# Optimization experiments

Hardware: AMD Instinct MI355X
Metric: run time of the kernel (lower is better)

## Reference

```python
import jax, jax.numpy as jnp
import numpy as np

EPS = 1e-05

def setup_inputs() -> dict:
    key = jax.random.key(0)
    inputs = jax.random.normal(key, (32, 512, 768), dtype=jnp.float32)
    return {"inputs": inputs}

def reference(inputs) -> jnp.ndarray:
    # position weight: L2 norm per token, w[b,l] = sqrt(1e-5 + sum_d x^2)
    w = jnp.sqrt(EPS + jnp.sum(inputs * inputs, axis=-1))  # [B, L]
    # output[b,d,e] = sum_l w[b,l] * x[b,l,d] * x[b,l,e]
    # fused weighted Gram matrix; never materializes [B,L,D,D]
    return jnp.einsum('bld,ble->bde', inputs * w[..., None], inputs)
```

## Files before the change

kernel.cpp:

```cpp
#include <hip/hip_runtime.h>
#include <hip/hip_bf16.h>

#define BATCH 32
#define LL 512
#define DD 768
#define EPSC 1e-5f

typedef __attribute__((ext_vector_type(8))) short bf16x8;
typedef __attribute__((ext_vector_type(4))) float f32x4;

__global__ __launch_bounds__(256) void k_scales(const float* __restrict__ x,
                                                float* __restrict__ s) {
    int wave = threadIdx.x >> 6;
    int lane = threadIdx.x & 63;
    int row = blockIdx.x * 4 + wave;
    const float4* xr = (const float4*)(x + (size_t)row * DD);
    float sum = 0.f;
#pragma unroll
    for (int i = 0; i < 3; i++) {
        float4 v = xr[lane + i * 64];
        sum += v.x * v.x + v.y * v.y + v.z * v.z + v.w * v.w;
    }
#pragma unroll
    for (int off = 32; off > 0; off >>= 1)
        sum += __shfl_xor(sum, off, 64);
    if (lane == 0) s[row] = sqrtf(sqrtf(EPSC + sum));
}

__global__ __launch_bounds__(256) void k_transpose(const float* __restrict__ x,
                                                   const float* __restrict__ s,
                                                   ushort* __restrict__ yt) {
    __shared__ float tile[64][65];
    __shared__ float svec[64];
    int b = blockIdx.z;
    int l0 = blockIdx.y * 64;
    int d0 = blockIdx.x * 64;
    int t = threadIdx.x;
    if (t < 64) svec[t] = s[b * LL + l0 + t];
    const float* xp = x + ((size_t)b * LL + l0) * DD + d0;
    int f = t & 15, lr0 = t >> 4;
#pragma unroll
    for (int r = 0; r < 4; r++) {
        int l = lr0 + r * 16;
        float4 v = *(const float4*)(xp + (size_t)l * DD + f * 4);
#pragma unroll
        for (int j = 0; j < 4; j++)
            tile[l][f * 4 + j] = ((const float*)&v)[j];
    }
    __syncthreads();
    ushort* yp = yt + ((size_t)b * DD + d0) * LL + l0;
    int lc = t & 7, dl0 = t >> 3;
#pragma unroll
    for (int it = 0; it < 2; it++) {
        int d = dl0 + it * 32;
        bf16x8 w;
#pragma unroll
        for (int j = 0; j < 8; j++) {
            int l = lc * 8 + j;
            float v = tile[l][d] * svec[l];
            __hip_bfloat16 h = __float2bfloat16(v);
            w[j] = *(short*)&h;
        }
        *(bf16x8*)(yp + (size_t)d * LL + lc * 8) = w;
    }
}

__global__ __launch_bounds__(256) void k_gemm(const ushort* __restrict__ yt,
                                              float* __restrict__ out) {
    __shared__ ushort At[2][64 * 32];
    __shared__ ushort Bt[2][64 * 32];
    int i = blockIdx.x;
    int xcd = i & 7, slot = i >> 3;
    int b = xcd + 8 * (slot / 78);
    int p = slot % 78;
    int t = p, tm = 0, rem = 12;
    while (t >= rem) { t -= rem; rem--; tm++; }
    int tn = tm + t;
    bool diag = (tm == tn);
    int m0 = tm * 64, n0 = tn * 64;
    int tid = threadIdx.x;
    int wave = tid >> 6, lane = tid & 63;
    int wr = wave >> 1, wc = wave & 1;
    const ushort* yb = yt + (size_t)b * DD * LL;

    f32x4 acc[2][2];
#pragma unroll
    for (int ii = 0; ii < 2; ii++)
#pragma unroll
        for (int j = 0; j < 2; j++) acc[ii][j] = (f32x4){0.f, 0.f, 0.f, 0.f};

    int srow = lane >> 2;
    int ssw = (srow ^ (srow >> 1)) & 3;
    int scol = ((lane & 3) ^ ssw) * 8;
    int rloc = wave * 16 + srow;
    const ushort* gA = yb + (size_t)(m0 + rloc) * LL + scol;
    const ushort* gB = yb + (size_t)(n0 + rloc) * LL + scol;
    int fr = lane & 15;
    int fsw = (fr ^ (fr >> 1)) & 3;
    int fslot = (lane >> 4) ^ fsw;

#define STAGE(buf, ks) do {                                                   \
        int k0_ = (ks) * 32;                                                  \
        __builtin_amdgcn_global_load_lds(                                     \
            (const __attribute__((address_space(1))) void*)(gA + k0_),        \
            (__attribute__((address_space(3))) void*)(At[buf] + wave * 16 * 32), \
            16, 0, 0);                                                        \
        if (!diag)                                                            \
            __builtin_amdgcn_global_load_lds(                                 \
                (const __attribute__((address_space(1))) void*)(gB + k0_),    \
                (__attribute__((address_space(3))) void*)(Bt[buf] + wave * 16 * 32), \
                16, 0, 0);                                                    \
    } while (0)

    STAGE(0, 0);
    __syncthreads();
    for (int ks = 0; ks < 16; ks++) {
        int cur = ks & 1;
        if (ks < 15) STAGE(cur ^ 1, ks + 1);
        const ushort* Ab = At[cur];
        const ushort* Bb = diag ? At[cur] : Bt[cur];
        bf16x8 afrag[2], bfrag[2];
#pragma unroll
        for (int ii = 0; ii < 2; ii++) {
            int m = wr * 32 + ii * 16 + fr;
            afrag[ii] = *(const bf16x8*)(Ab + m * 32 + fslot * 8);
            int n = wc * 32 + ii * 16 + fr;
            bfrag[ii] = *(const bf16x8*)(Bb + n * 32 + fslot * 8);
        }
#pragma unroll
        for (int ii = 0; ii < 2; ii++)
#pragma unroll
            for (int j = 0; j < 2; j++)
                acc[ii][j] = __builtin_amdgcn_mfma_f32_16x16x32_bf16(
                    afrag[ii], bfrag[j], acc[ii][j], 0, 0, 0);
        if (ks < 15) __syncthreads();
    }
#undef STAGE

    float* op = out + (size_t)b * DD * DD;
#pragma unroll
    for (int ii = 0; ii < 2; ii++) {
        int colb = m0 + wr * 32 + ii * 16 + (lane >> 4) * 4;
#pragma unroll
        for (int j = 0; j < 2; j++) {
            int row = n0 + wc * 32 + j * 16 + fr;
            float4 v = {acc[ii][j][0], acc[ii][j][1], acc[ii][j][2], acc[ii][j][3]};
            *(float4*)(op + (size_t)row * DD + colb) = v;
        }
    }
    if (!diag) {
#pragma unroll
        for (int ii = 0; ii < 2; ii++) {
            int mbase = m0 + wr * 32 + ii * 16 + (lane >> 4) * 4;
#pragma unroll
            for (int j = 0; j < 2; j++) {
                int n = n0 + wc * 32 + j * 16 + fr;
#pragma unroll
                for (int r = 0; r < 4; r++)
                    op[(size_t)(mbase + r) * DD + n] = acc[ii][j][r];
            }
        }
    }
}

extern "C" void kernel_launch(void* const* d_in, const int* in_sizes, int n_in,
                              void* d_out, int out_size, void* d_ws, size_t ws_size,
                              hipStream_t stream) {
    const float* x = (const float*)d_in[0];
    float* s = (float*)d_ws;
    ushort* yt = (ushort*)((char*)d_ws + 65536);

    k_scales<<<dim3((BATCH * LL) / 4), 256, 0, stream>>>(x, s);
    k_transpose<<<dim3(DD / 64, LL / 64, BATCH), 256, 0, stream>>>(x, s, yt);
    k_gemm<<<dim3(78 * BATCH), 256, 0, stream>>>(yt, (float*)d_out);
}
```

Measured before the change: 137.8 us.

## Fuse norm and transpose kernels; double GEMM K-tile to 64

The row-norm scale computation is merged into the transpose kernel. Each block now handles 64 tokens across all 768 features, computing the scales locally and looping over 12 feature tiles. The GEMM K-step grows from 32 to 64 with a new XOR swizzle, which halves the number of barriers and loop iterations. The risk is the prep kernel: it drops to only 256 blocks, each running a long serial loop, which lowers parallelism.

```diff
diff --git a/kernel.cpp b/kernel.cpp
--- a/kernel.cpp
+++ b/kernel.cpp
@@ -9,66 +9,66 @@
 typedef __attribute__((ext_vector_type(8))) short bf16x8;
 typedef __attribute__((ext_vector_type(4))) float f32x4;
 
-__global__ __launch_bounds__(256) void k_scales(const float* __restrict__ x,
-                                                float* __restrict__ s) {
-    int wave = threadIdx.x >> 6;
-    int lane = threadIdx.x & 63;
-    int row = blockIdx.x * 4 + wave;
-    const float4* xr = (const float4*)(x + (size_t)row * DD);
-    float sum = 0.f;
-#pragma unroll
-    for (int i = 0; i < 3; i++) {
-        float4 v = xr[lane + i * 64];
-        sum += v.x * v.x + v.y * v.y + v.z * v.z + v.w * v.w;
-    }
-#pragma unroll
-    for (int off = 32; off > 0; off >>= 1)
-        sum += __shfl_xor(sum, off, 64);
-    if (lane == 0) s[row] = sqrtf(sqrtf(EPSC + sum));
-}
-
-__global__ __launch_bounds__(256) void k_transpose(const float* __restrict__ x,
-                                                   const float* __restrict__ s,
-                                                   ushort* __restrict__ yt) {
+__global__ __launch_bounds__(256) void k_prep(const float* __restrict__ x,
+                                              ushort* __restrict__ yt) {
     __shared__ float tile[64][65];
     __shared__ float svec[64];
-    int b = blockIdx.z;
-    int l0 = blockIdx.y * 64;
-    int d0 = blockIdx.x * 64;
+    int lb = blockIdx.x;
+    int b = blockIdx.y;
+    int l0 = lb * 64;
     int t = threadIdx.x;
-    if (t < 64) svec[t] = s[b * LL + l0 + t];
-    const float* xp = x + ((size_t)b * LL + l0) * DD + d0;
-    int f = t & 15, lr0 = t >> 4;
-#pragma unroll
-    for (int r = 0; r < 4; r++) {
-        int l = lr0 + r * 16;
-        float4 v = *(const float4*)(xp + (size_t)l * DD + f * 4);
-#pragma unroll
-        for (int j = 0; j < 4; j++)
-            tile[l][f * 4 + j] = ((const float*)&v)[j];
+
+    {
+        int r = t >> 2, q = t & 3;
+        const float4* xr = (const float4*)(x + ((size_t)b * LL + l0 + r) * DD) + q * 48;
+        float sum = 0.f;
+#pragma unroll 8
+        for (int i = 0; i < 48; i++) {
+            float4 v = xr[i];
+            sum += v.x * v.x + v.y * v.y + v.z * v.z + v.w * v.w;
+        }
+        sum += __shfl_xor(sum, 1, 64);
+        sum += __shfl_xor(sum, 2, 64);
+        if (q == 0) svec[r] = sqrtf(sqrtf(EPSC + sum));
     }
     __syncthreads();
-    ushort* yp = yt + ((size_t)b * DD + d0) * LL + l0;
+
+    const float* xb = x + ((size_t)b * LL + l0) * DD;
+    int f = t & 15, lr0 = t >> 4;
     int lc = t & 7, dl0 = t >> 3;
+    for (int dt = 0; dt < 12; dt++) {
+        int d0 = dt * 64;
 #pragma unroll
-    for (int it = 0; it < 2; it++) {
-        int d = dl0 + it * 32;
-        bf16x8 w;
+        for (int r = 0; r < 4; r++) {
+            int l = lr0 + r * 16;
+            float4 v = *(const float4*)(xb + (size_t)l * DD + d0 + f * 4);
 #pragma unroll
-        for (int j = 0; j < 8; j++) {
-            int l = lc * 8 + j;
-            float v = tile[l][d] * svec[l];
-            __hip_bfloat16 h = __float2bfloat16(v);
-            w[j] = *(short*)&h;
+            for (int j = 0; j < 4; j++)
+                tile[l][f * 4 + j] = ((const float*)&v)[j];
         }
-        *(bf16x8*)(yp + (size_t)d * LL + lc * 8) = w;
+        __syncthreads();
+        ushort* yp = yt + ((size_t)b * DD + d0) * LL + l0;
+#pragma unroll
+        for (int it = 0; it < 2; it++) {
+            int d = dl0 + it * 32;
+            bf16x8 w;
+#pragma unroll
+            for (int j = 0; j < 8; j++) {
+                int l = lc * 8 + j;
+                float v = tile[l][d] * svec[l];
+                __hip_bfloat16 h = __float2bfloat16(v);
+                w[j] = *(short*)&h;
+            }
+            *(bf16x8*)(yp + (size_t)d * LL + lc * 8) = w;
+        }
+        __syncthreads();
     }
 }
 
 __global__ __launch_bounds__(256) void k_gemm(const ushort* __restrict__ yt,
                                               float* __restrict__ out) {
-    __shared__ ushort At[2][64 * 32];
-    __shared__ ushort Bt[2][64 * 32];
+    __shared__ ushort At[2][64 * 64];
+    __shared__ ushort Bt[2][64 * 64];
     int i = blockIdx.x;
     int xcd = i & 7, slot = i >> 3;
     int b = xcd + 8 * (slot / 78);
@@ -89,51 +89,69 @@
 #pragma unroll
         for (int j = 0; j < 2; j++) acc[ii][j] = (f32x4){0.f, 0.f, 0.f, 0.f};
 
-    int srow = lane >> 2;
-    int ssw = (srow ^ (srow >> 1)) & 3;
-    int scol = ((lane & 3) ^ ssw) * 8;
-    int rloc = wave * 16 + srow;
-    const ushort* gA = yb + (size_t)(m0 + rloc) * LL + scol;
-    const ushort* gB = yb + (size_t)(n0 + rloc) * LL + scol;
-    int fr = lane & 15;
-    int fsw = (fr ^ (fr >> 1)) & 3;
-    int fslot = (lane >> 4) ^ fsw;
+    int s0 = tid, s1 = 256 + tid;
+    int sr0 = s0 >> 3, sc0 = (s0 & 7) ^ (sr0 & 7);
+    int sr1 = s1 >> 3, sc1 = (s1 & 7) ^ (sr1 & 7);
+    const ushort* gA0 = yb + (size_t)(m0 + sr0) * LL + sc0 * 8;
+    const ushort* gA1 = yb + (size_t)(m0 + sr1) * LL + sc1 * 8;
+    const ushort* gB0 = yb + (size_t)(n0 + sr0) * LL + sc0 * 8;
+    const ushort* gB1 = yb + (size_t)(n0 + sr1) * LL + sc1 * 8;
+    int ldsOff0 = (0 * 256 + wave * 64) * 8;
+    int ldsOff1 = (1 * 256 + wave * 64) * 8;
+
+    int fr = lane & 15, ks4 = lane >> 4;
 
 #define STAGE(buf, ks) do {                                                   \
-        int k0_ = (ks) * 32;                                                  \
+        int k0_ = (ks) * 64;                                                  \
         __builtin_amdgcn_global_load_lds(                                     \
-            (const __attribute__((address_space(1))) void*)(gA + k0_),        \
-            (__attribute__((address_space(3))) void*)(At[buf] + wave * 16 * 32), \
+            (const __attribute__((address_space(1))) void*)(gA0 + k0_),       \
+            (__attribute__((address_space(3))) void*)(At[buf] + ldsOff0),     \
             16, 0, 0);                                                        \
-        if (!diag)                                                            \
+        __builtin_amdgcn_global_load_lds(                                     \
+            (const __attribute__((address_space(1))) void*)(gA1 + k0_),       \
+            (__attribute__((address_space(3))) void*)(At[buf] + ldsOff1),     \
+            16, 0, 0);                                                        \
+        if (!diag) {                                                          \
             __builtin_amdgcn_global_load_lds(                                 \
-                (const __attribute__((address_space(1))) void*)(gB + k0_),    \
-                (__attribute__((address_space(3))) void*)(Bt[buf] + wave * 16 * 32), \
+                (const __attribute__((address_space(1))) void*)(gB0 + k0_),   \
+                (__attribute__((address_space(3))) void*)(Bt[buf] + ldsOff0), \
                 16, 0, 0);                                                    \
+            __builtin_amdgcn_global_load_lds(                                 \
+                (const __attribute__((address_space(1))) void*)(gB1 + k0_),   \
+                (__attribute__((address_space(3))) void*)(Bt[buf] + ldsOff1), \
+                16, 0, 0);                                                    \
+        }                                                                     \
     } while (0)
 
     STAGE(0, 0);
     __syncthreads();
-    for (int ks = 0; ks < 16; ks++) {
+    for (int ks = 0; ks < 8; ks++) {
         int cur = ks & 1;
-        if (ks < 15) STAGE(cur ^ 1, ks + 1);
+        if (ks < 7) STAGE(cur ^ 1, ks + 1);
         const ushort* Ab = At[cur];
         const ushort* Bb = diag ? At[cur] : Bt[cur];
-        bf16x8 afrag[2], bfrag[2];
+        bf16x8 af[2][2], bf[2][2];
 #pragma unroll
         for (int ii = 0; ii < 2; ii++) {
-            int m = wr * 32 + ii * 16 + fr;
-            afrag[ii] = *(const bf16x8*)(Ab + m * 32 + fslot * 8);
-            int n = wc * 32 + ii * 16 + fr;
-            bfrag[ii] = *(const bf16x8*)(Bb + n * 32 + fslot * 8);
+            int mr = wr * 32 + ii * 16 + fr;
+            int nr = wc * 32 + ii * 16 + fr;
+#pragma unroll
+            for (int h = 0; h < 2; h++) {
+                int slm = ((h * 4 + ks4) ^ (mr & 7)) * 8;
+                int sln = ((h * 4 + ks4) ^ (nr & 7)) * 8;
+                af[ii][h] = *(const bf16x8*)(Ab + mr * 64 + slm);
+                bf[ii][h] = *(const bf16x8*)(Bb + nr * 64 + sln);
+            }
         }
 #pragma unroll
         for (int ii = 0; ii < 2; ii++)
 #pragma unroll
             for (int j = 0; j < 2; j++)
-                acc[ii][j] = __builtin_amdgcn_mfma_f32_16x16x32_bf16(
-                    afrag[ii], bfrag[j], acc[ii][j], 0, 0, 0);
-        if (ks < 15) __syncthreads();
+#pragma unroll
+                for (int h = 0; h < 2; h++)
+                    acc[ii][j] = __builtin_amdgcn_mfma_f32_16x16x32_bf16(
+                        af[ii][h], bf[j][h], acc[ii][j], 0, 0, 0);
+        if (ks < 7) __syncthreads();
     }
 #undef STAGE
 
@@ -167,10 +185,8 @@
                               void* d_out, int out_size, void* d_ws, size_t ws_size,
                               hipStream_t stream) {
     const float* x = (const float*)d_in[0];
-    float* s = (float*)d_ws;
-    ushort* yt = (ushort*)((char*)d_ws + 65536);
+    ushort* yt = (ushort*)d_ws;
 
-    k_scales<<<dim3((BATCH * LL) / 4), 256, 0, stream>>>(x, s);
-    k_transpose<<<dim3(DD / 64, LL / 64, BATCH), 256, 0, stream>>>(x, s, yt);
+    k_prep<<<dim3(LL / 64, BATCH), 256, 0, stream>>>(x, yt);
     k_gemm<<<dim3(78 * BATCH), 256, 0, stream>>>(yt, (float*)d_out);
 }
```

New measurement: 130.8 us. -5.0%, faster.
